# Optimization experiments

Measured on AMD Instinct MI355X. Metric: run time of the kernel, lower is better.

The kernel has to match this reference:

```python
import jax, jax.numpy as jnp
import numpy as np

K_DELTA = 2.0
K_AN = 2.0
N_CLASSES = 32


def _masked_mean(x, mask):
    m = mask.astype(x.dtype)
    return jnp.sum(x * m) / jnp.maximum(jnp.sum(m), 1.0)


def setup_inputs() -> dict:
    key = jax.random.key(0)
    k1, k2 = jax.random.split(key)
    logits = jax.random.normal(k1, (384, 1024), dtype=jnp.float32)
    labels = jax.random.randint(k2, (384,), 0, N_CLASSES)
    return {"logits": logits, "labels": labels}


def reference(logits, labels):
    # Faithful jit-safe translation: torch.where / torch.unique produce
    # dynamic-shaped index lists; here we return the equivalent boolean
    # masks over the full triplet / pair space instead.
    N = labels.shape[0]
    x = jax.lax.stop_gradient(logits)  # logits.detach()
    x = x / jnp.linalg.norm(x, axis=1, keepdims=True)  # F.normalize p=2 dim=1
    mat = -(x @ x.T)  # negative cosine similarity, symmetric [N, N]

    sames = labels[:, None] == labels[None, :]
    diffs = ~sames
    sames = sames & ~jnp.eye(N, dtype=bool)  # fill_diagonal_(0)
    # triplet validity mask over (anchor, positive, negative)
    trip = sames[:, :, None] & diffs[:, None, :]  # [N, N, N]

    # delta[a, p, n] = an_dist - ap_dist
    delta = mat[:, None, :] - mat[:, :, None]  # [N, N, N]

    # --- calc_loss_an branch: unique (anchor, negative) pairs ---
    # a pair (a, n) appears in some triplet iff diffs[a, n] and anchor a has
    # at least one positive; unique_filter canonicalizes to (min, max).
    has_pos = jnp.any(sames, axis=1)  # [N]
    upper = jnp.triu(jnp.ones((N, N), dtype=bool), k=1)
    pair_mask = upper & diffs & (has_pos[:, None] | has_pos[None, :])
    an_mean = _masked_mean(mat, pair_mask)
    beta = 1.0 + (-an_mean - 1.0) / K_AN  # self.update(an_dist_unique, 'an')
    an_pairs = pair_mask & (-mat >= beta)

    # --- epsilon update + semi-hard triplet selection ---
    eps = jnp.clip(_masked_mean(delta, trip) / K_DELTA, 0.0, 0.5)
    cond = trip & (delta <= eps) & (delta > 0.0)  # semi-hard

    return cond, an_pairs, eps, beta
```

## Files before the change

kernel.cpp:

```cpp
#include <hip/hip_runtime.h>
#include <stdint.h>

#define N 384
#define D 1024
#define N2 (N * N)
static constexpr size_t N3 = (size_t)N * N2;

static constexpr size_t PART_OFF = 0;
static constexpr size_t INVN_OFF = 4718592;
static constexpr size_t TN_OFF   = 4721664;
static constexpr size_t TC_OFF   = 4724736;
static constexpr size_t ANS_OFF  = 4727808;
static constexpr size_t ANC_OFF  = 4730880;
static constexpr size_t HP_OFF   = 4733952;
static constexpr size_t SYNC_OFF = 4735488;

static constexpr int GEMM_BLOCKS = 576;
static constexpr int NORM_BLOCKS = 96;
static constexpr int FILL_BLOCKS = 2048;
static constexpr int FILL_F4     = 14192640;
static constexpr int TAIL_BLOCKS = 192;

#define AGT __HIP_MEMORY_SCOPE_AGENT

__global__ __launch_bounds__(256) void k_mega(const float* __restrict__ x,
                                              double* __restrict__ part,
                                              double* __restrict__ invn,
                                              int* __restrict__ sync,
                                              float4* __restrict__ outv) {
  __shared__ double As[64][32];
  __shared__ double Bs[64][32];
  int b = blockIdx.x;
  int t = threadIdx.x;

  if (b >= GEMM_BLOCKS + NORM_BLOCKS) {
    int i = (b - GEMM_BLOCKS - NORM_BLOCKS) * 256 + t;
    const int stride = FILL_BLOCKS * 256;
    const float4 z = make_float4(0.f, 0.f, 0.f, 0.f);
    for (; i < FILL_F4; i += stride) outv[i] = z;
    return;
  }
  if (b >= GEMM_BLOCKS) {
    if (b == GEMM_BLOCKS && t == 0)
      __hip_atomic_store(sync, 0, __ATOMIC_RELAXED, AGT);
    int w = t >> 6, lane = t & 63;
    int a = (b - GEMM_BLOCKS) * 4 + w;
    const float4* row = (const float4*)(x + (size_t)a * D);
    double s = 0.0;
#pragma unroll
    for (int j = 0; j < 4; ++j) {
      float4 v = row[lane + 64 * j];
      double dx = v.x, dy = v.y, dz = v.z, dw = v.w;
      s += dx * dx + dy * dy + dz * dz + dw * dw;
    }
#pragma unroll
    for (int m = 32; m; m >>= 1) s += __shfl_xor(s, m, 64);
    if (lane == 0) invn[a] = 1.0 / sqrt(s);
    return;
  }

  int bz = b / 144, rem = b % 144;
  int m0 = (rem % 12) * 32, n0 = (rem / 12) * 32, k0 = bz * 256;
  int tm = t & 15, tn = t >> 4;
  double a00 = 0, a01 = 0, a10 = 0, a11 = 0;
  for (int kc = 0; kc < 4; ++kc) {
    int kbase = k0 + kc * 64;
#pragma unroll
    for (int h = 0; h < 2; ++h) {
      int f = t + h * 256;
      int m = f & 31, kq = f >> 5;
      float4 va = *(const float4*)(x + (size_t)(m0 + m) * D + kbase + kq * 4);
      As[kq * 4 + 0][m] = (double)va.x; As[kq * 4 + 1][m] = (double)va.y;
      As[kq * 4 + 2][m] = (double)va.z; As[kq * 4 + 3][m] = (double)va.w;
      float4 vb = *(const float4*)(x + (size_t)(n0 + m) * D + kbase + kq * 4);
      Bs[kq * 4 + 0][m] = (double)vb.x; Bs[kq * 4 + 1][m] = (double)vb.y;
      Bs[kq * 4 + 2][m] = (double)vb.z; Bs[kq * 4 + 3][m] = (double)vb.w;
    }
    __syncthreads();
#pragma unroll 8
    for (int k = 0; k < 64; ++k) {
      double ax = As[k][2 * tm], ay = As[k][2 * tm + 1];
      double bx = Bs[k][2 * tn], by = Bs[k][2 * tn + 1];
      a00 = fma(ax, bx, a00);
      a01 = fma(ax, by, a01);
      a10 = fma(ay, bx, a10);
      a11 = fma(ay, by, a11);
    }
    __syncthreads();
  }
  double* o = part + (size_t)bz * N2;
  int r0 = m0 + 2 * tm, c0 = n0 + 2 * tn;
  o[(size_t)r0 * N + c0]           = a00;
  o[(size_t)r0 * N + c0 + 1]       = a01;
  o[(size_t)(r0 + 1) * N + c0]     = a10;
  o[(size_t)(r0 + 1) * N + c0 + 1] = a11;
}

__global__ __launch_bounds__(384) void k_tail(const double* __restrict__ part,
                                              const double* __restrict__ invn,
                                              const int* __restrict__ labels,
                                              double* __restrict__ tn,
                                              double* __restrict__ tc,
                                              double* __restrict__ ans,
                                              double* __restrict__ anc,
                                              int* __restrict__ hp,
                                              int* __restrict__ sync,
                                              float* __restrict__ out) {
  __shared__ int labs[N];
  __shared__ int hist[32];
  __shared__ double cw[6][6];
  __shared__ double matX[2][N];
  __shared__ int hpL[N];
  __shared__ int list[N];
  __shared__ int cnt;
  __shared__ double sEps, sBeta;
  int t = threadIdx.x;
  int w = t >> 6, lane = t & 63;
  if (t < 32) hist[t] = 0;
  labs[t] = labels[t];
  __syncthreads();
  atomicAdd(&hist[labs[t] & 31], 1);
  __syncthreads();

  for (int half = 0; half < 2; ++half) {
    int a = blockIdx.x + half * TAIL_BLOCKS;
    int la = labs[a];
    size_t idx = (size_t)a * N + t;
    double s = part[idx];
    s += part[(size_t)N2 + idx];
    s += part[2 * (size_t)N2 + idx];
    s += part[3 * (size_t)N2 + idx];
    double m = -(s * (invn[a] * invn[t]));
    matX[half][t] = m;
    bool same = (labs[t] == la) && (t != a);
    bool diff = (labs[t] != la);
    bool hpa = hist[la] >= 2;
    bool hpt = hist[labs[t]] >= 2;
    bool anm = (t > a) && diff && (hpa || hpt);

    double q[6];
    q[0] = same ? m : 0.0;
    q[1] = same ? 1.0 : 0.0;
    q[2] = diff ? m : 0.0;
    q[3] = diff ? 1.0 : 0.0;
    q[4] = anm ? m : 0.0;
    q[5] = anm ? 1.0 : 0.0;
#pragma unroll
    for (int i = 0; i < 6; ++i) {
#pragma unroll
      for (int s2 = 32; s2; s2 >>= 1) q[i] += __shfl_xor(q[i], s2, 64);
    }
    if (lane == 0) {
#pragma unroll
      for (int i = 0; i < 6; ++i) cw[w][i] = q[i];
    }
    __syncthreads();
    if (t == 0) {
      double r[6];
#pragma unroll
      for (int i = 0; i < 6; ++i) {
        double s3 = 0.0;
        for (int ww = 0; ww < 6; ++ww) s3 += cw[ww][i];
        r[i] = s3;
      }
      __hip_atomic_store(&tn[a],  r[2] * r[1] - r[0] * r[3], __ATOMIC_RELAXED, AGT);
      __hip_atomic_store(&tc[a],  r[1] * r[3], __ATOMIC_RELAXED, AGT);
      __hip_atomic_store(&ans[a], r[4], __ATOMIC_RELAXED, AGT);
      __hip_atomic_store(&anc[a], r[5], __ATOMIC_RELAXED, AGT);
      __hip_atomic_store(&hp[a],  hpa ? 1 : 0, __ATOMIC_RELAXED, AGT);
    }
    __syncthreads();
  }

  if (t == 0) {
    __threadfence();
    atomicAdd(sync, 1);
    while (__hip_atomic_load(sync, __ATOMIC_RELAXED, AGT) < TAIL_BLOCKS) {}
    __threadfence();
  }
  __syncthreads();

  hpL[t] = __hip_atomic_load(&hp[t], __ATOMIC_RELAXED, AGT);
  if (t < 64) {
    double vtn = 0, vtc = 0, vas = 0, vac = 0;
#pragma unroll
    for (int j = 0; j < 6; ++j) {
      int idx = t + 64 * j;
      vtn += __hip_atomic_load(&tn[idx],  __ATOMIC_RELAXED, AGT);
      vtc += __hip_atomic_load(&tc[idx],  __ATOMIC_RELAXED, AGT);
      vas += __hip_atomic_load(&ans[idx], __ATOMIC_RELAXED, AGT);
      vac += __hip_atomic_load(&anc[idx], __ATOMIC_RELAXED, AGT);
    }
#pragma unroll
    for (int s = 32; s; s >>= 1) {
      vtn += __shfl_xor(vtn, s, 64);
      vtc += __shfl_xor(vtc, s, 64);
      vas += __shfl_xor(vas, s, 64);
      vac += __shfl_xor(vac, s, 64);
    }
    if (t == 0) {
      double an_mean = vas / fmax(vac, 1.0);
      double beta = 1.0 + ((-an_mean) - 1.0) / 2.0;
      double em = vtn / fmax(vtc, 1.0);
      double eps = em / 2.0;
      eps = eps < 0.0 ? 0.0 : (eps > 0.5 ? 0.5 : eps);
      sEps = eps;
      sBeta = beta;
      if (blockIdx.x == 0) {
        out[N3 + N2]     = (float)eps;
        out[N3 + N2 + 1] = (float)beta;
      }
    }
  }
  __syncthreads();
  double eps = sEps, beta = sBeta;

  for (int half = 0; half < 2; ++half) {
    int a = blockIdx.x + half * TAIL_BLOCKS;
    int la = labs[a];
    int hpa = hpL[a];
    if (t == 0) cnt = 0;
    __syncthreads();
    if (labs[t] == la && t != a) list[atomicAdd(&cnt, 1)] = t;
    __syncthreads();
    if (t < 96) {
      int b0 = t * 4;
      float r[4];
#pragma unroll
      for (int j = 0; j < 4; ++j) {
        int b = b0 + j;
        bool pm = (a < b) && (labs[b] != la) && (hpa || hpL[b]);
        r[j] = (pm && (-matX[half][b] >= beta)) ? 1.0f : 0.0f;
      }
      *((float4*)(out + N3 + (size_t)a * N + b0)) =
          make_float4(r[0], r[1], r[2], r[3]);
    }
    int nc = cnt;
    for (int base = 0; base < nc; base += 4) {
      int rr = base + (t / 96);
      if (rr < nc) {
        int p = list[rr];
        double mp = matX[half][p];
        int n0 = (t % 96) * 4;
        float r[4];
#pragma unroll
        for (int j = 0; j < 4; ++j) {
          int n = n0 + j;
          double d = matX[half][n] - mp;
          r[j] = ((labs[n] != la) && (d > 0.0) && (d <= eps)) ? 1.0f : 0.0f;
        }
        *((float4*)(out + (size_t)a * N2 + (size_t)p * N + n0)) =
            make_float4(r[0], r[1], r[2], r[3]);
      }
    }
    __syncthreads();
  }
}

extern "C" void kernel_launch(void* const* d_in, const int* in_sizes, int n_in,
                              void* d_out, int out_size, void* d_ws, size_t ws_size,
                              hipStream_t stream) {
  const float* logits = (const float*)d_in[0];
  const int* labels = (const int*)d_in[1];
  float* out = (float*)d_out;
  char* ws = (char*)d_ws;
  double* part = (double*)(ws + PART_OFF);
  double* invn = (double*)(ws + INVN_OFF);
  double* tn   = (double*)(ws + TN_OFF);
  double* tc   = (double*)(ws + TC_OFF);
  double* ans  = (double*)(ws + ANS_OFF);
  double* anc  = (double*)(ws + ANC_OFF);
  int* hp      = (int*)(ws + HP_OFF);
  int* sync    = (int*)(ws + SYNC_OFF);

  k_mega<<<dim3(GEMM_BLOCKS + NORM_BLOCKS + FILL_BLOCKS), dim3(256), 0,
           stream>>>(logits, part, invn, sync, (float4*)out);
  k_tail<<<dim3(TAIL_BLOCKS), dim3(384), 0, stream>>>(
      part, invn, labels, tn, tc, ans, anc, hp, sync, out);
}
```

Before: 57.80 us.

## Map one anchor per tail block with 256 threads and sleep in grid barrier

The tail kernel now launches 384 blocks of 256 threads, one anchor row per block, instead of 192 blocks of 384 threads that each processed two anchors. Per-thread loops cover the 384 columns, and the semi-hard triplet write loop now uses 192 threads covering two positive rows per iteration. The spin-wait barrier drops its threadfences and adds s_sleep between polls. The aim is more parallelism across CUs and less per-block serial work, at the cost of a grid barrier over more blocks, which relies on all 384 blocks being co-resident. Removing the fences weakens the memory-ordering guarantees of the barrier.

```diff
diff --git a/kernel.cpp b/kernel.cpp
--- a/kernel.cpp
+++ b/kernel.cpp
@@ -19,7 +19,7 @@
 static constexpr int NORM_BLOCKS = 96;
 static constexpr int FILL_BLOCKS = 2048;
 static constexpr int FILL_F4     = 14192640;
-static constexpr int TAIL_BLOCKS = 192;
+static constexpr int TAIL_BLOCKS = 384;
 
 #define AGT __HIP_MEMORY_SCOPE_AGENT
 
@@ -61,7 +61,7 @@
 
   int bz = b / 144, rem = b % 144;
   int m0 = (rem % 12) * 32, n0 = (rem / 12) * 32, k0 = bz * 256;
-  int tm = t & 15, tn = t >> 4;
+  int tm = t & 15, tn_ = t >> 4;
   double a00 = 0, a01 = 0, a10 = 0, a11 = 0;
   for (int kc = 0; kc < 4; ++kc) {
     int kbase = k0 + kc * 64;
@@ -80,7 +80,7 @@
 #pragma unroll 8
     for (int k = 0; k < 64; ++k) {
       double ax = As[k][2 * tm], ay = As[k][2 * tm + 1];
-      double bx = Bs[k][2 * tn], by = Bs[k][2 * tn + 1];
+      double bx = Bs[k][2 * tn_], by = Bs[k][2 * tn_ + 1];
       a00 = fma(ax, bx, a00);
       a01 = fma(ax, by, a01);
       a10 = fma(ay, bx, a10);
@@ -89,14 +89,14 @@
     __syncthreads();
   }
   double* o = part + (size_t)bz * N2;
-  int r0 = m0 + 2 * tm, c0 = n0 + 2 * tn;
+  int r0 = m0 + 2 * tm, c0 = n0 + 2 * tn_;
   o[(size_t)r0 * N + c0]           = a00;
   o[(size_t)r0 * N + c0 + 1]       = a01;
   o[(size_t)(r0 + 1) * N + c0]     = a10;
   o[(size_t)(r0 + 1) * N + c0 + 1] = a11;
 }
 
-__global__ __launch_bounds__(384) void k_tail(const double* __restrict__ part,
+__global__ __launch_bounds__(256) void k_tail(const double* __restrict__ part,
                                               const double* __restrict__ invn,
                                               const int* __restrict__ labels,
                                               double* __restrict__ tn,
@@ -108,79 +108,83 @@
                                               float* __restrict__ out) {
   __shared__ int labs[N];
   __shared__ int hist[32];
-  __shared__ double cw[6][6];
-  __shared__ double matX[2][N];
+  __shared__ double cw[4][6];
+  __shared__ double matA[N];
   __shared__ int hpL[N];
   __shared__ int list[N];
   __shared__ int cnt;
   __shared__ double sEps, sBeta;
-  int t = threadIdx.x;
+  int a = blockIdx.x, t = threadIdx.x;
+
+  for (int i = t; i < N; i += 256) labs[i] = labels[i];
+  if (t < 32) hist[t] = 0;
+  if (t == 0) cnt = 0;
+  __syncthreads();
+  for (int i = t; i < N; i += 256) atomicAdd(&hist[labs[i] & 31], 1);
+  __syncthreads();
+  int la = labs[a];
+  bool hpa = hist[la] >= 2;
+  double ia = invn[a];
+  double q[6] = {0, 0, 0, 0, 0, 0};
+#pragma unroll
+  for (int rep = 0; rep < 2; ++rep) {
+    int c = t + rep * 256;
+    if (c < N) {
+      size_t idx = (size_t)a * N + c;
+      double s = part[idx];
+      s += part[(size_t)N2 + idx];
+      s += part[2 * (size_t)N2 + idx];
+      s += part[3 * (size_t)N2 + idx];
+      double m = -(s * (ia * invn[c]));
+      matA[c] = m;
+      bool same = (labs[c] == la) && (c != a);
+      bool diff = (labs[c] != la);
+      bool hpt = hist[labs[c]] >= 2;
+      bool anm = (c > a) && diff && (hpa || hpt);
+      q[0] += same ? m : 0.0;
+      q[1] += same ? 1.0 : 0.0;
+      q[2] += diff ? m : 0.0;
+      q[3] += diff ? 1.0 : 0.0;
+      q[4] += anm ? m : 0.0;
+      q[5] += anm ? 1.0 : 0.0;
+    }
+  }
   int w = t >> 6, lane = t & 63;
-  if (t < 32) hist[t] = 0;
-  labs[t] = labels[t];
-  __syncthreads();
-  atomicAdd(&hist[labs[t] & 31], 1);
-  __syncthreads();
-
-  for (int half = 0; half < 2; ++half) {
-    int a = blockIdx.x + half * TAIL_BLOCKS;
-    int la = labs[a];
-    size_t idx = (size_t)a * N + t;
-    double s = part[idx];
-    s += part[(size_t)N2 + idx];
-    s += part[2 * (size_t)N2 + idx];
-    s += part[3 * (size_t)N2 + idx];
-    double m = -(s * (invn[a] * invn[t]));
-    matX[half][t] = m;
-    bool same = (labs[t] == la) && (t != a);
-    bool diff = (labs[t] != la);
-    bool hpa = hist[la] >= 2;
-    bool hpt = hist[labs[t]] >= 2;
-    bool anm = (t > a) && diff && (hpa || hpt);
-
-    double q[6];
-    q[0] = same ? m : 0.0;
-    q[1] = same ? 1.0 : 0.0;
-    q[2] = diff ? m : 0.0;
-    q[3] = diff ? 1.0 : 0.0;
-    q[4] = anm ? m : 0.0;
-    q[5] = anm ? 1.0 : 0.0;
+#pragma unroll
+  for (int i = 0; i < 6; ++i) {
+#pragma unroll
+    for (int s2 = 32; s2; s2 >>= 1) q[i] += __shfl_xor(q[i], s2, 64);
+  }
+  if (lane == 0) {
+#pragma unroll
+    for (int i = 0; i < 6; ++i) cw[w][i] = q[i];
+  }
+  __syncthreads();
+  if (t == 0) {
+    double r[6];
 #pragma unroll
     for (int i = 0; i < 6; ++i) {
-#pragma unroll
-      for (int s2 = 32; s2; s2 >>= 1) q[i] += __shfl_xor(q[i], s2, 64);
-    }
-    if (lane == 0) {
-#pragma unroll
-      for (int i = 0; i < 6; ++i) cw[w][i] = q[i];
-    }
-    __syncthreads();
-    if (t == 0) {
-      double r[6];
-#pragma unroll
-      for (int i = 0; i < 6; ++i) {
-        double s3 = 0.0;
-        for (int ww = 0; ww < 6; ++ww) s3 += cw[ww][i];
-        r[i] = s3;
-      }
-      __hip_atomic_store(&tn[a],  r[2] * r[1] - r[0] * r[3], __ATOMIC_RELAXED, AGT);
-      __hip_atomic_store(&tc[a],  r[1] * r[3], __ATOMIC_RELAXED, AGT);
-      __hip_atomic_store(&ans[a], r[4], __ATOMIC_RELAXED, AGT);
-      __hip_atomic_store(&anc[a], r[5], __ATOMIC_RELAXED, AGT);
-      __hip_atomic_store(&hp[a],  hpa ? 1 : 0, __ATOMIC_RELAXED, AGT);
-    }
-    __syncthreads();
-  }
+      double s3 = 0.0;
+      for (int ww = 0; ww < 4; ++ww) s3 += cw[ww][i];
+      r[i] = s3;
+    }
+    __hip_atomic_store(&tn[a],  r[2] * r[1] - r[0] * r[3], __ATOMIC_RELAXED, AGT);
+    __hip_atomic_store(&tc[a],  r[1] * r[3], __ATOMIC_RELAXED, AGT);
+    __hip_atomic_store(&ans[a], r[4], __ATOMIC_RELAXED, AGT);
+    __hip_atomic_store(&anc[a], r[5], __ATOMIC_RELAXED, AGT);
+    __hip_atomic_store(&hp[a],  hpa ? 1 : 0, __ATOMIC_RELAXED, AGT);
+  }
+  __syncthreads();
 
   if (t == 0) {
-    __threadfence();
     atomicAdd(sync, 1);
-    while (__hip_atomic_load(sync, __ATOMIC_RELAXED, AGT) < TAIL_BLOCKS) {}
-    __threadfence();
-  }
-  __syncthreads();
-
-  hpL[t] = __hip_atomic_load(&hp[t], __ATOMIC_RELAXED, AGT);
+    while (__hip_atomic_load(sync, __ATOMIC_RELAXED, AGT) < TAIL_BLOCKS)
+      __builtin_amdgcn_s_sleep(8);
+  }
+  __syncthreads();
+
+  for (int i = t; i < N; i += 256)
+    hpL[i] = __hip_atomic_load(&hp[i], __ATOMIC_RELAXED, AGT);
   if (t < 64) {
     double vtn = 0, vtc = 0, vas = 0, vac = 0;
 #pragma unroll
@@ -206,7 +210,7 @@
       eps = eps < 0.0 ? 0.0 : (eps > 0.5 ? 0.5 : eps);
       sEps = eps;
       sBeta = beta;
-      if (blockIdx.x == 0) {
+      if (a == 0) {
         out[N3 + N2]     = (float)eps;
         out[N3 + N2 + 1] = (float)beta;
       }
@@ -214,46 +218,41 @@
   }
   __syncthreads();
   double eps = sEps, beta = sBeta;
-
-  for (int half = 0; half < 2; ++half) {
-    int a = blockIdx.x + half * TAIL_BLOCKS;
-    int la = labs[a];
-    int hpa = hpL[a];
-    if (t == 0) cnt = 0;
-    __syncthreads();
-    if (labs[t] == la && t != a) list[atomicAdd(&cnt, 1)] = t;
-    __syncthreads();
-    if (t < 96) {
-      int b0 = t * 4;
+  int hpa_i = hpL[a];
+
+  for (int i = t; i < N; i += 256) {
+    if (labs[i] == la && i != a) list[atomicAdd(&cnt, 1)] = i;
+  }
+  __syncthreads();
+  if (t < 96) {
+    int b0 = t * 4;
+    float r[4];
+#pragma unroll
+    for (int j = 0; j < 4; ++j) {
+      int b = b0 + j;
+      bool pm = (a < b) && (labs[b] != la) && (hpa_i || hpL[b]);
+      r[j] = (pm && (-matA[b] >= beta)) ? 1.0f : 0.0f;
+    }
+    *((float4*)(out + N3 + (size_t)a * N + b0)) =
+        make_float4(r[0], r[1], r[2], r[3]);
+  }
+  int nc = cnt;
+  for (int base = 0; base < nc; base += 2) {
+    int rr = base + (t / 96);
+    if (t < 192 && rr < nc) {
+      int p = list[rr];
+      double mp = matA[p];
+      int n0 = (t % 96) * 4;
       float r[4];
 #pragma unroll
       for (int j = 0; j < 4; ++j) {
-        int b = b0 + j;
-        bool pm = (a < b) && (labs[b] != la) && (hpa || hpL[b]);
-        r[j] = (pm && (-matX[half][b] >= beta)) ? 1.0f : 0.0f;
+        int n = n0 + j;
+        double d = matA[n] - mp;
+        r[j] = ((labs[n] != la) && (d > 0.0) && (d <= eps)) ? 1.0f : 0.0f;
       }
-      *((float4*)(out + N3 + (size_t)a * N + b0)) =
+      *((float4*)(out + (size_t)a * N2 + (size_t)p * N + n0)) =
           make_float4(r[0], r[1], r[2], r[3]);
     }
-    int nc = cnt;
-    for (int base = 0; base < nc; base += 4) {
-      int rr = base + (t / 96);
-      if (rr < nc) {
-        int p = list[rr];
-        double mp = matX[half][p];
-        int n0 = (t % 96) * 4;
-        float r[4];
-#pragma unroll
-        for (int j = 0; j < 4; ++j) {
-          int n = n0 + j;
-          double d = matX[half][n] - mp;
-          r[j] = ((labs[n] != la) && (d > 0.0) && (d <= eps)) ? 1.0f : 0.0f;
-        }
-        *((float4*)(out + (size_t)a * N2 + (size_t)p * N + n0)) =
-            make_float4(r[0], r[1], r[2], r[3]);
-      }
-    }
-    __syncthreads();
   }
 }
 
@@ -275,6 +274,6 @@
 
   k_mega<<<dim3(GEMM_BLOCKS + NORM_BLOCKS + FILL_BLOCKS), dim3(256), 0,
            stream>>>(logits, part, invn, sync, (float4*)out);
-  k_tail<<<dim3(TAIL_BLOCKS), dim3(384), 0, stream>>>(
+  k_tail<<<dim3(TAIL_BLOCKS), dim3(256), 0, stream>>>(
       part, invn, labels, tn, tc, ans, anc, hp, sync, out);
 }
```

Result: no change. 58.19 us (+0.7%).
